# Optimization experiments

Hardware: AMD Instinct MI355X
Metric: run time of the kernel (lower is better)

## Reference

```python
import jax, jax.numpy as jnp
import numpy as np

BN_EPS = 1e-5

def _bn_eval(x, g, b, m, v):
    # BatchNorm1d in eval mode with running stats
    return (x - m) * (g / jnp.sqrt(v + BN_EPS)) + b

def _gcn_layer(x, adj, w, b):
    # D^-0.5 A D^-0.5 (X W) + b  (same math as diag(d^-0.5) @ adj @ diag(d^-0.5))
    deg = adj.sum(axis=1)
    dis = deg ** -0.5
    xw = x @ w
    return dis[:, None] * (adj @ (dis[:, None] * xw)) + b

def setup_inputs() -> dict:
    key = jax.random.key(0)
    ks = jax.random.split(key, 8)
    N, F, E, H, G, C = 16384, 1024, 256, 256, 128, 10
    def xavier(k, i, o):
        s = float(np.sqrt(6.0 / (i + o)))
        return jax.random.uniform(k, (i, o), jnp.float32, -s, s)
    return {
        "feature": jax.random.uniform(ks[0], (N, F), jnp.float32),
        "adj": jax.random.uniform(ks[1], (N, N), jnp.float32),
        "enc_w1": xavier(ks[2], F, 512), "enc_b1": jnp.zeros((512,), jnp.float32),
        "bn1_g": jnp.ones((512,), jnp.float32), "bn1_b": jnp.zeros((512,), jnp.float32),
        "bn1_m": jnp.zeros((512,), jnp.float32), "bn1_v": jnp.ones((512,), jnp.float32),
        "enc_w2": xavier(ks[3], 512, E), "enc_b2": jnp.zeros((E,), jnp.float32),
        "bn2_g": jnp.ones((E,), jnp.float32), "bn2_b": jnp.zeros((E,), jnp.float32),
        "bn2_m": jnp.zeros((E,), jnp.float32), "bn2_v": jnp.ones((E,), jnp.float32),
        "gcn1_w": xavier(ks[4], E, H), "gcn1_b": jnp.zeros((H,), jnp.float32),
        "gcn2_w": xavier(ks[5], H, G), "gcn2_b": jnp.zeros((G,), jnp.float32),
        "cls_w": xavier(ks[6], G, C), "cls_b": jnp.zeros((C,), jnp.float32),
    }

def reference(feature, adj, enc_w1, enc_b1, bn1_g, bn1_b, bn1_m, bn1_v,
              enc_w2, enc_b2, bn2_g, bn2_b, bn2_m, bn2_v,
              gcn1_w, gcn1_b, gcn2_w, gcn2_b, cls_w, cls_b):
    # encoder.encode (eval: dropout off, BN running stats)
    h = jax.nn.relu(_bn_eval(feature @ enc_w1 + enc_b1, bn1_g, bn1_b, bn1_m, bn1_v))
    h = jax.nn.relu(_bn_eval(h @ enc_w2 + enc_b2, bn2_g, bn2_b, bn2_m, bn2_v))
    h = jax.nn.relu(_gcn_layer(h, adj, gcn1_w, gcn1_b))
    h = jax.nn.relu(_gcn_layer(h, adj, gcn2_w, gcn2_b))
    out = jax.nn.sigmoid(h @ cls_w + cls_b)
    return jnp.clip(out, 1e-10, 1 - 1e-10)
```

## Files before the change

kernel.cpp:

```cpp
#include <hip/hip_runtime.h>
#include <stdint.h>

typedef unsigned short u16;
typedef unsigned int u32;
typedef __attribute__((ext_vector_type(4))) float f32x4;
typedef __attribute__((ext_vector_type(16))) float f32x16;
typedef __attribute__((ext_vector_type(8))) short s16x8;
typedef __attribute__((ext_vector_type(4))) short s16x4;
typedef __attribute__((ext_vector_type(2))) unsigned int u32x2;
typedef __attribute__((ext_vector_type(4))) unsigned int u32x4;
typedef __attribute__((ext_vector_type(8))) int i32x8;

__device__ __forceinline__ u16 f2bf(float x){
  unsigned u = __builtin_bit_cast(unsigned, x);
  u += 0x7fffu + ((u >> 16) & 1u);
  return (u16)(u >> 16);
}
__device__ __forceinline__ float bf2f(u16 b){
  return __builtin_bit_cast(float, (unsigned)b << 16);
}
__device__ __forceinline__ u32 pk_fp8x4(float a, float b, float c, float d){
  int w = 0;
  w = __builtin_amdgcn_cvt_pk_fp8_f32(a, b, w, false);
  w = __builtin_amdgcn_cvt_pk_fp8_f32(c, d, w, true);
  return (u32)w;
}


__global__ void bn_prep_kernel(const float* __restrict__ g, const float* __restrict__ b,
                               const float* __restrict__ m, const float* __restrict__ v,
                               const float* __restrict__ lin_b,
                               float* __restrict__ s, float* __restrict__ bb, int n){
  int i = blockIdx.x * 256 + threadIdx.x;
  if (i < n){
    float sc = g[i] * rsqrtf(v[i] + 1e-5f);
    s[i] = sc;
    bb[i] = (lin_b[i] - m[i]) * sc + b[i];
  }
}

__global__ __launch_bounds__(256) void tcvtT_kernel(const float* __restrict__ src,
                                                    u16* __restrict__ dst, int K, int N){
  __shared__ float t[32][33];
  int tx = threadIdx.x & 31, ty = threadIdx.x >> 5;
  int n0 = blockIdx.x * 32, k0 = blockIdx.y * 32;
  #pragma unroll
  for (int i = 0; i < 4; i++)
    t[ty + 8 * i][tx] = src[(size_t)(k0 + ty + 8 * i) * N + n0 + tx];
  __syncthreads();
  #pragma unroll
  for (int i = 0; i < 4; i++)
    dst[(size_t)(n0 + ty + 8 * i) * K + k0 + tx] = f2bf(t[tx][ty + 8 * i]);
}

__global__ __launch_bounds__(256) void enc1_deg_kernel(
    const float* __restrict__ feature, const u16* __restrict__ w1t,
    u16* __restrict__ h1, const float* __restrict__ cs, const float* __restrict__ cb,
    const float* __restrict__ adj, unsigned char* __restrict__ adj8,
    float* __restrict__ dis)
{
  constexpr int BM = 128, BN = 256, BK = 64, WM = 2, WN = 2;
  constexpr int M = 16384, N = 512, K = 1024, NADJ = 16384;
  constexpr int WTM = BM / WM, WTN = BN / WN, FM = WTM / 16, FN = WTN / 16;
  constexpr int AIT = (BM * BK) / (256 * 4);
  constexpr int BIT = (BN * BK) / (256 * 8);

  __shared__ __align__(16) char smem[BM * BK * 2 + BN * BK * 2];

  if (blockIdx.x >= 256){
    int row = blockIdx.x - 256;
    const float* rp = adj + (size_t)row * NADJ;
    unsigned char* wp = adj8 + (size_t)row * NADJ;
    float s = 0.f;
    #pragma unroll
    for (int it = 0; it < 4; ++it){
      const float* p = rp + it * 4096 + threadIdx.x * 16;
      f32x4 v[4];
      #pragma unroll
      for (int j = 0; j < 4; ++j) v[j] = *(const f32x4*)(p + 4 * j);
      u32x4 o;
      #pragma unroll
      for (int j = 0; j < 4; ++j){
        s += (v[j][0] + v[j][1]) + (v[j][2] + v[j][3]);
        o[j] = pk_fp8x4(v[j][0], v[j][1], v[j][2], v[j][3]);
      }
      *(u32x4*)(wp + it * 4096 + threadIdx.x * 16) = o;
    }
    #pragma unroll
    for (int d = 32; d > 0; d >>= 1) s += __shfl_down(s, d, 64);
    float* ps = (float*)smem;
    if ((threadIdx.x & 63) == 0) ps[threadIdx.x >> 6] = s;
    __syncthreads();
    if (threadIdx.x == 0) dis[row] = rsqrtf((ps[0] + ps[1]) + (ps[2] + ps[3]));
    return;
  }

  u16* As = (u16*)smem;
  u16* Bs = (u16*)(smem + BM * BK * 2);
  const int tid = threadIdx.x;
  const int lane = tid & 63;
  const int wid = tid >> 6;
  const int wr = wid / WN;
  const int wc = wid % WN;
  const int bm = (blockIdx.x & 127) * BM;
  const int bn = (blockIdx.x >> 7) * BN;

  f32x4 arf[AIT];
  s16x8 brb[BIT];

  auto load_tiles = [&](int k0){
    #pragma unroll
    for (int i = 0; i < AIT; i++){
      int e = (i * 256 + tid) * 4; int r = e / BK, c = e % BK;
      arf[i] = *(const f32x4*)(feature + (size_t)(bm + r) * K + k0 + c);
    }
    #pragma unroll
    for (int i = 0; i < BIT; i++){
      int e = (i * 256 + tid) * 8; int r = e / BK, c = e % BK;
      brb[i] = *(const s16x8*)(w1t + (size_t)(bn + r) * K + k0 + c);
    }
  };
  auto store_tiles = [&](){
    char* Ac = (char*)As; char* Bc = (char*)Bs;
    #pragma unroll
    for (int i = 0; i < AIT; i++){
      int e = (i * 256 + tid) * 4; int r = e / BK, c = e % BK;
      int off = ((r * BK + c) * 2) ^ ((r & 7) << 4);
      s16x4 o;
      o[0] = (short)f2bf(arf[i][0]); o[1] = (short)f2bf(arf[i][1]);
      o[2] = (short)f2bf(arf[i][2]); o[3] = (short)f2bf(arf[i][3]);
      *(s16x4*)(Ac + off) = o;
    }
    #pragma unroll
    for (int i = 0; i < BIT; i++){
      int e = (i * 256 + tid) * 8; int r = e / BK, c = e % BK;
      int off = ((r * BK + c) * 2) ^ ((r & 7) << 4);
      *(s16x8*)(Bc + off) = brb[i];
    }
  };

  f32x4 acc[FM][FN];
  #pragma unroll
  for (int m = 0; m < FM; m++)
    #pragma unroll
    for (int n = 0; n < FN; n++)
      acc[m][n] = (f32x4){0.f, 0.f, 0.f, 0.f};

  const int arow0 = wr * WTM + (lane & 15);
  const int brow0 = wc * WTN + (lane & 15);
  const int kof = (lane >> 4) * 8;

  load_tiles(0);
  for (int kt = 0; kt < K / BK; ++kt){
    __syncthreads();
    store_tiles();
    __syncthreads();
    if (kt + 1 < K / BK) load_tiles((kt + 1) * BK);
    const char* Ac = (const char*)As;
    const char* Bc = (const char*)Bs;
    #pragma unroll
    for (int ks = 0; ks < BK / 32; ++ks){
      s16x8 af[FM], bfr[FN];
      #pragma unroll
      for (int m = 0; m < FM; m++){
        int r = arow0 + m * 16;
        af[m] = *(const s16x8*)(Ac + (((r * BK + ks * 32 + kof) * 2) ^ ((r & 7) << 4)));
      }
      #pragma unroll
      for (int n = 0; n < FN; n++){
        int r = brow0 + n * 16;
        bfr[n] = *(const s16x8*)(Bc + (((r * BK + ks * 32 + kof) * 2) ^ ((r & 7) << 4)));
      }
      #pragma unroll
      for (int m = 0; m < FM; m++)
        #pragma unroll
        for (int n = 0; n < FN; n++)
          acc[m][n] = __builtin_amdgcn_mfma_f32_16x16x32_bf16(af[m], bfr[n], acc[m][n], 0, 0, 0);
    }
  }
  #pragma unroll
  for (int m = 0; m < FM; m++){
    #pragma unroll
    for (int n = 0; n < FN; n++){
      int col = bn + wc * WTN + n * 16 + (lane & 15);
      int row0 = bm + wr * WTM + m * 16 + (lane >> 4) * 4;
      #pragma unroll
      for (int r4 = 0; r4 < 4; r4++){
        float vv = fmaxf(acc[m][n][r4] * cs[col] + cb[col], 0.f);
        h1[(size_t)(row0 + r4) * N + col] = f2bf(vv);
      }
    }
  }
}

__global__ __launch_bounds__(256) void gcn_reduce_kernel(const float* __restrict__ part,
                                                         const float* __restrict__ dis,
                                                         const float* __restrict__ b,
                                                         u16* __restrict__ out,
                                                         int N, size_t MN, float oscale){
  size_t e4 = ((size_t)blockIdx.x * 256 + threadIdx.x) * 4;
  int row = (int)(e4 / N);
  int col = (int)(e4 % N);
  f32x4 s = *(const f32x4*)(part + e4);
  s += *(const f32x4*)(part + MN + e4);
  float dr = dis[row] * oscale;
  s16x4 o;
  #pragma unroll
  for (int j = 0; j < 4; j++){
    float vv = fmaxf(dr * s[j] + b[col + j], 0.f);
    o[j] = (short)f2bf(vv);
  }
  *(s16x4*)(out + e4) = o;
}

__global__ __launch_bounds__(256) void cls_kernel(const u16* __restrict__ h4,
                                                  const float* __restrict__ w,
                                                  const float* __restrict__ b,
                                                  float* __restrict__ out, int M){
  __shared__ float ws_[128 * 10];
  __shared__ float bs_[10];
  for (int i = threadIdx.x; i < 1280; i += 256) ws_[i] = w[i];
  if (threadIdx.x < 10) bs_[threadIdx.x] = b[threadIdx.x];
  __syncthreads();
  int row = blockIdx.x * 256 + threadIdx.x;
  if (row >= M) return;
  const u16* hp = h4 + (size_t)row * 128;
  float acc[10];
  #pragma unroll
  for (int c = 0; c < 10; c++) acc[c] = bs_[c];
  #pragma unroll
  for (int k8 = 0; k8 < 128; k8 += 8){
    s16x8 hv = *(const s16x8*)(hp + k8);
    #pragma unroll
    for (int j = 0; j < 8; j++){
      float h = bf2f((u16)hv[j]);
      #pragma unroll
      for (int c = 0; c < 10; c++) acc[c] = fmaf(h, ws_[(k8 + j) * 10 + c], acc[c]);
    }
  }
  #pragma unroll
  for (int c = 0; c < 10; c++){
    float sg = 1.f / (1.f + expf(-acc[c]));
    sg = fminf(fmaxf(sg, 1e-10f), 1.f - 1e-10f);
    out[(size_t)row * 10 + c] = sg;
  }
}

template<int BM, int BN>
__global__ __launch_bounds__(512, 1)
void gemm_mx(const unsigned char* __restrict__ A8, const unsigned char* __restrict__ B8,
             float* __restrict__ P, int M, int N, int K, int Ksub)
{
  constexpr int BK = 128;
  constexpr int AT = BM * BK;
  constexpr int BT = BN * BK;
  constexpr int AIT = AT / (512 * 16);
  constexpr int BIT = BT / (512 * 16);
  constexpr int WM = 2, WN = 4;
  constexpr int WTM = BM / WM;
  constexpr int WTN = BN / WN;
  constexpr int FM = WTM / 32;
  constexpr int FN = WTN / 32;
  static_assert(AIT >= 1 && BIT >= 1, "staging");

  __shared__ __align__(16) char LDS[2 * (AT + BT)];

  const int tid = threadIdx.x;
  const int lane = tid & 63;
  const int wid = tid >> 6;
  const int wr = wid >> 2;
  const int wc = wid & 3;
  const int bm = blockIdx.x * BM;
  const int kz = blockIdx.z * Ksub;

  auto stage = [&](int half, int k0){
    char* ab = LDS + half * (AT + BT);
    #pragma unroll
    for (int i = 0; i < AIT; i++){
      int e = (i * 512 + tid) * 16;
      int r = e >> 7, c = e & 127;
      int cc = c ^ ((r & 7) << 4);
      const unsigned char* g = A8 + (size_t)(bm + r) * K + k0 + cc;
      __builtin_amdgcn_global_load_lds((const __attribute__((address_space(1))) unsigned int*)g,
          (__attribute__((address_space(3))) unsigned int*)(ab + e), 16, 0, 0);
    }
    char* bb = ab + AT;
    #pragma unroll
    for (int i = 0; i < BIT; i++){
      int e = (i * 512 + tid) * 16;
      int r = e >> 7, c = e & 127;
      int cc = c ^ ((r & 7) << 4);
      const unsigned char* g = B8 + (size_t)r * K + k0 + cc;
      __builtin_amdgcn_global_load_lds((const __attribute__((address_space(1))) unsigned int*)g,
          (__attribute__((address_space(3))) unsigned int*)(bb + e), 16, 0, 0);
    }
  };

  f32x16 acc[FM][FN];
  #pragma unroll
  for (int m = 0; m < FM; m++)
    #pragma unroll
    for (int n = 0; n < FN; n++)
      #pragma unroll
      for (int i = 0; i < 16; i++)
        acc[m][n][i] = 0.f;

  const int nk = Ksub / BK;
  stage(0, kz);
  for (int kt = 0; kt < nk; ++kt){
    __syncthreads();
    if (kt + 1 < nk) stage((kt + 1) & 1, kz + (kt + 1) * BK);
    const char* ab = LDS + (kt & 1) * (AT + BT);
    const char* bb = ab + AT;
    #pragma unroll
    for (int ks = 0; ks < 2; ks++){
      const int c0 = ks * 64 + (lane >> 5) * 32;
      i32x8 af[FM], bf_[FN];
      #pragma unroll
      for (int m = 0; m < FM; m++){
        int r = wr * WTM + m * 32 + (lane & 31);
        int sw = (r & 7) << 4;
        int o = r * BK + c0;
        u32x4 lo = *(const u32x4*)(ab + (o ^ sw));
        u32x4 hi = *(const u32x4*)(ab + ((o + 16) ^ sw));
        af[m][0] = lo[0]; af[m][1] = lo[1]; af[m][2] = lo[2]; af[m][3] = lo[3];
        af[m][4] = hi[0]; af[m][5] = hi[1]; af[m][6] = hi[2]; af[m][7] = hi[3];
      }
      #pragma unroll
      for (int n = 0; n < FN; n++){
        int r = wc * WTN + n * 32 + (lane & 31);
        int sw = (r & 7) << 4;
        int o = r * BK + c0;
        u32x4 lo = *(const u32x4*)(bb + (o ^ sw));
        u32x4 hi = *(const u32x4*)(bb + ((o + 16) ^ sw));
        bf_[n][0] = lo[0]; bf_[n][1] = lo[1]; bf_[n][2] = lo[2]; bf_[n][3] = lo[3];
        bf_[n][4] = hi[0]; bf_[n][5] = hi[1]; bf_[n][6] = hi[2]; bf_[n][7] = hi[3];
      }
      #pragma unroll
      for (int m = 0; m < FM; m++)
        #pragma unroll
        for (int n = 0; n < FN; n++)
          acc[m][n] = __builtin_amdgcn_mfma_scale_f32_32x32x64_f8f6f4(
              af[m], bf_[n], acc[m][n], 0, 0, 0, 0x7F7F7F7F, 0, 0x7F7F7F7F);
    }
  }

  float* Pz = P + (size_t)blockIdx.z * M * N;
  #pragma unroll
  for (int m = 0; m < FM; m++){
    #pragma unroll
    for (int n = 0; n < FN; n++){
      int colg = wc * WTN + n * 32 + (lane & 31);
      int rbase = bm + wr * WTM + m * 32 + (lane >> 5) * 4;
      #pragma unroll
      for (int i = 0; i < 16; i++){
        int rowg = rbase + (i & 3) + 8 * (i >> 2);
        Pz[(size_t)rowg * N + colg] = acc[m][n][i];
      }
    }
  }
}

enum { EPI_BNRELU = 0, EPI_SCALET = 1 };

template<int BM, int BN, int BK, int WM, int WN, int EPI>
__global__ __launch_bounds__(WM*WN*64, 1)
void gemm_k(const u16* __restrict__ Ab, const u16* __restrict__ Bb,
            void* __restrict__ Cp, int M, int N, int K,
            const float* __restrict__ cs, const float* __restrict__ cb,
            const float* __restrict__ rs, float oscale)
{
  constexpr int NT = WM * WN * 64;
  constexpr int WTM = BM / WM;
  constexpr int WTN = BN / WN;
  constexpr int FM = WTM / 16;
  constexpr int FN = WTN / 16;
  constexpr int AIT = (BM * BK) / (NT * 8);
  constexpr int BIT = (BN * BK) / (NT * 8);
  static_assert((BM * BK) % (NT * 8) == 0, "A staging");
  static_assert((BN * BK) % (NT * 8) == 0, "B staging");

  __shared__ u16 As[BM * BK];
  __shared__ u16 Bs[BN * BK];

  const int tid = threadIdx.x;
  const int lane = tid & 63;
  const int wid = tid >> 6;
  const int wr = wid / WN;
  const int wc = wid % WN;
  const int bm = blockIdx.x * BM;
  const int bn = blockIdx.y * BN;

  s16x8 arb[AIT];
  s16x8 brb[BIT];

  auto load_tiles = [&](int k0){
    #pragma unroll
    for (int i = 0; i < AIT; i++){
      int e = (i * NT + tid) * 8; int r = e / BK, c = e % BK;
      arb[i] = *(const s16x8*)(Ab + (size_t)(bm + r) * K + k0 + c);
    }
    #pragma unroll
    for (int i = 0; i < BIT; i++){
      int e = (i * NT + tid) * 8; int r = e / BK, c = e % BK;
      brb[i] = *(const s16x8*)(Bb + (size_t)(bn + r) * K + k0 + c);
    }
  };
  auto store_tiles = [&](){
    char* Ac = (char*)As; char* Bc = (char*)Bs;
    #pragma unroll
    for (int i = 0; i < AIT; i++){
      int e = (i * NT + tid) * 8; int r = e / BK, c = e % BK;
      int off = ((r * BK + c) * 2) ^ ((r & 7) << 4);
      *(s16x8*)(Ac + off) = arb[i];
    }
    #pragma unroll
    for (int i = 0; i < BIT; i++){
      int e = (i * NT + tid) * 8; int r = e / BK, c = e % BK;
      int off = ((r * BK + c) * 2) ^ ((r & 7) << 4);
      *(s16x8*)(Bc + off) = brb[i];
    }
  };

  f32x4 acc[FM][FN];
  #pragma unroll
  for (int m = 0; m < FM; m++)
    #pragma unroll
    for (int n = 0; n < FN; n++)
      acc[m][n] = (f32x4){0.f, 0.f, 0.f, 0.f};

  const int arow0 = wr * WTM + (lane & 15);
  const int brow0 = wc * WTN + (lane & 15);
  const int kof = (lane >> 4) * 8;

  const int nk = K / BK;
  load_tiles(0);
  for (int kt = 0; kt < nk; ++kt){
    __syncthreads();
    store_tiles();
    __syncthreads();
    if (kt + 1 < nk) load_tiles((kt + 1) * BK);
    const char* Ac = (const char*)As;
    const char* Bc = (const char*)Bs;
    #pragma unroll
    for (int ks = 0; ks < BK / 32; ++ks){
      s16x8 af[FM], bfr[FN];
      #pragma unroll
      for (int m = 0; m < FM; m++){
        int r = arow0 + m * 16;
        af[m] = *(const s16x8*)(Ac + (((r * BK + ks * 32 + kof) * 2) ^ ((r & 7) << 4)));
      }
      #pragma unroll
      for (int n = 0; n < FN; n++){
        int r = brow0 + n * 16;
        bfr[n] = *(const s16x8*)(Bc + (((r * BK + ks * 32 + kof) * 2) ^ ((r & 7) << 4)));
      }
      #pragma unroll
      for (int m = 0; m < FM; m++)
        #pragma unroll
        for (int n = 0; n < FN; n++)
          acc[m][n] = __builtin_amdgcn_mfma_f32_16x16x32_bf16(af[m], bfr[n], acc[m][n], 0, 0, 0);
    }
  }

  #pragma unroll
  for (int m = 0; m < FM; m++){
    #pragma unroll
    for (int n = 0; n < FN; n++){
      int col = bn + wc * WTN + n * 16 + (lane & 15);
      int row0 = bm + wr * WTM + m * 16 + (lane >> 4) * 4;
      if constexpr (EPI == EPI_SCALET){
        float v0 = acc[m][n][0] * rs[row0 + 0] * oscale;
        float v1 = acc[m][n][1] * rs[row0 + 1] * oscale;
        float v2 = acc[m][n][2] * rs[row0 + 2] * oscale;
        float v3 = acc[m][n][3] * rs[row0 + 3] * oscale;
        *(u32*)((unsigned char*)Cp + (size_t)col * M + row0) = pk_fp8x4(v0, v1, v2, v3);
      } else {
        #pragma unroll
        for (int r4 = 0; r4 < 4; r4++){
          int row = row0 + r4;
          float vv = fmaxf(acc[m][n][r4] * cs[col] + cb[col], 0.f);
          ((u16*)Cp)[(size_t)row * N + col] = f2bf(vv);
        }
      }
    }
  }
}


extern "C" void kernel_launch(void* const* d_in, const int* in_sizes, int n_in,
                              void* d_out, int out_size, void* d_ws, size_t ws_size,
                              hipStream_t stream)
{
  (void)in_sizes; (void)n_in; (void)out_size; (void)ws_size;
  const float* feature = (const float*)d_in[0];
  const float* adj     = (const float*)d_in[1];
  const float* enc_w1  = (const float*)d_in[2];
  const float* enc_b1  = (const float*)d_in[3];
  const float* bn1_g   = (const float*)d_in[4];
  const float* bn1_b   = (const float*)d_in[5];
  const float* bn1_m   = (const float*)d_in[6];
  const float* bn1_v   = (const float*)d_in[7];
  const float* enc_w2  = (const float*)d_in[8];
  const float* enc_b2  = (const float*)d_in[9];
  const float* bn2_g   = (const float*)d_in[10];
  const float* bn2_b   = (const float*)d_in[11];
  const float* bn2_m   = (const float*)d_in[12];
  const float* bn2_v   = (const float*)d_in[13];
  const float* gcn1_w  = (const float*)d_in[14];
  const float* gcn1_b  = (const float*)d_in[15];
  const float* gcn2_w  = (const float*)d_in[16];
  const float* gcn2_b  = (const float*)d_in[17];
  const float* cls_w   = (const float*)d_in[18];
  const float* cls_b   = (const float*)d_in[19];
  float* out = (float*)d_out;

  const int NN = 16384, F = 1024, H1 = 512, E = 256, H = 256, G = 128;
  const float SC = 256.f, SCI = 1.f / 256.f;

  char* ws = (char*)d_ws;
  size_t off = 0;
  auto alloc = [&](size_t bytes) -> char* {
    char* p = ws + off; off += (bytes + 255) & ~(size_t)255; return p;
  };
  float* dis = (float*)alloc((size_t)NN * 4);
  float* s1  = (float*)alloc((size_t)H1 * 4);
  float* bb1 = (float*)alloc((size_t)H1 * 4);
  float* s2  = (float*)alloc((size_t)E * 4);
  float* bb2 = (float*)alloc((size_t)E * 4);
  u16* w1t = (u16*)alloc((size_t)H1 * F * 2);
  u16* w2t = (u16*)alloc((size_t)E * H1 * 2);
  u16* g1t = (u16*)alloc((size_t)H * E * 2);
  u16* g2t = (u16*)alloc((size_t)G * H * 2);
  u16* h1  = (u16*)alloc((size_t)NN * H1 * 2);
  u16* h2  = (u16*)alloc((size_t)NN * E * 2);
  unsigned char* tT  = (unsigned char*)alloc((size_t)E * NN);
  u16* h3  = (u16*)alloc((size_t)NN * H * 2);
  unsigned char* t2T = (unsigned char*)alloc((size_t)G * NN);
  u16* h4  = (u16*)alloc((size_t)NN * G * 2);
  float* part = (float*)alloc((size_t)2 * NN * H * 4);
  unsigned char* adj8 = (unsigned char*)alloc((size_t)NN * NN);

  bn_prep_kernel<<<(H1 + 255) / 256, 256, 0, stream>>>(bn1_g, bn1_b, bn1_m, bn1_v, enc_b1, s1, bb1, H1);
  bn_prep_kernel<<<(E + 255) / 256, 256, 0, stream>>>(bn2_g, bn2_b, bn2_m, bn2_v, enc_b2, s2, bb2, E);
  tcvtT_kernel<<<dim3(H1/32, F/32), 256, 0, stream>>>(enc_w1, w1t, F, H1);
  tcvtT_kernel<<<dim3(E/32, H1/32), 256, 0, stream>>>(enc_w2, w2t, H1, E);
  tcvtT_kernel<<<dim3(H/32, E/32), 256, 0, stream>>>(gcn1_w, g1t, E, H);
  tcvtT_kernel<<<dim3(G/32, H/32), 256, 0, stream>>>(gcn2_w, g2t, H, G);

  enc1_deg_kernel<<<256 + NN, 256, 0, stream>>>(feature, w1t, h1, s1, bb1, adj, adj8, dis);

  gemm_k<128,128,64,2,2,EPI_BNRELU><<<dim3(NN/128, E/128), 256, 0, stream>>>(
      h1, w2t, h2, NN, E, H1, s2, bb2, nullptr, 1.f);
  gemm_k<128,128,64,2,2,EPI_SCALET><<<dim3(NN/128, H/128), 256, 0, stream>>>(
      h2, g1t, tT, NN, H, E, nullptr, nullptr, dis, SC);
  gemm_mx<128,256><<<dim3(NN/128, 1, 2), 512, 0, stream>>>(
      adj8, tT, part, NN, H, NN, NN/2);
  gcn_reduce_kernel<<<(NN * H) / 1024, 256, 0, stream>>>(
      part, dis, gcn1_b, h3, H, (size_t)NN * H, SCI);
  gemm_k<64,128,64,2,2,EPI_SCALET><<<dim3(NN/64, G/128), 256, 0, stream>>>(
      h3, g2t, t2T, NN, G, H, nullptr, nullptr, dis, SC);
  gemm_mx<128,128><<<dim3(NN/128, 1, 2), 512, 0, stream>>>(
      adj8, t2T, part, NN, G, NN, NN/2);
  gcn_reduce_kernel<<<(NN * G) / 1024, 256, 0, stream>>>(
      part, dis, gcn2_b, h4, G, (size_t)NN * G, SCI);
  cls_kernel<<<NN/256, 256, 0, stream>>>(h4, cls_w, cls_b, out, NN);
}
```

Baseline: 520.4 us.

## Fuse prep, small GEMMs, split-K reductions and classifier into fewer kernels

```diff
diff --git a/kernel.cpp b/kernel.cpp
--- a/kernel.cpp
+++ b/kernel.cpp
@@ -27,11 +27,26 @@
 }
 
 
-__global__ void bn_prep_kernel(const float* __restrict__ g, const float* __restrict__ b,
-                               const float* __restrict__ m, const float* __restrict__ v,
-                               const float* __restrict__ lin_b,
-                               float* __restrict__ s, float* __restrict__ bb, int n){
-  int i = blockIdx.x * 256 + threadIdx.x;
+__device__ __forceinline__ void tcvtT_dev(const float* __restrict__ src, u16* __restrict__ dst,
+                                          int K, int N, int bx, int by, char* smem){
+  float (*t)[33] = (float (*)[33])smem;
+  int tx = threadIdx.x & 31, ty = threadIdx.x >> 5;
+  int n0 = bx * 32, k0 = by * 32;
+  #pragma unroll
+  for (int i = 0; i < 4; i++)
+    t[ty + 8 * i][tx] = src[(size_t)(k0 + ty + 8 * i) * N + n0 + tx];
+  __syncthreads();
+  #pragma unroll
+  for (int i = 0; i < 4; i++)
+    dst[(size_t)(n0 + ty + 8 * i) * K + k0 + tx] = f2bf(t[tx][ty + 8 * i]);
+}
+
+__device__ __forceinline__ void bn_dev(const float* __restrict__ g, const float* __restrict__ b,
+                                       const float* __restrict__ m, const float* __restrict__ v,
+                                       const float* __restrict__ lin_b,
+                                       float* __restrict__ s, float* __restrict__ bb,
+                                       int n, int blk){
+  int i = blk * 256 + threadIdx.x;
   if (i < n){
     float sc = g[i] * rsqrtf(v[i] + 1e-5f);
     s[i] = sc;
@@ -39,33 +54,47 @@
   }
 }
 
-__global__ __launch_bounds__(256) void tcvtT_kernel(const float* __restrict__ src,
-                                                    u16* __restrict__ dst, int K, int N){
-  __shared__ float t[32][33];
-  int tx = threadIdx.x & 31, ty = threadIdx.x >> 5;
-  int n0 = blockIdx.x * 32, k0 = blockIdx.y * 32;
-  #pragma unroll
-  for (int i = 0; i < 4; i++)
-    t[ty + 8 * i][tx] = src[(size_t)(k0 + ty + 8 * i) * N + n0 + tx];
-  __syncthreads();
-  #pragma unroll
-  for (int i = 0; i < 4; i++)
-    dst[(size_t)(n0 + ty + 8 * i) * K + k0 + tx] = f2bf(t[tx][ty + 8 * i]);
+__global__ __launch_bounds__(256) void prep0_kernel(
+    const float* __restrict__ enc_w1, u16* __restrict__ w1t,
+    const float* __restrict__ g, const float* __restrict__ b,
+    const float* __restrict__ m, const float* __restrict__ v,
+    const float* __restrict__ lin_b, float* __restrict__ s1, float* __restrict__ bb1)
+{
+  __shared__ char smem[32 * 33 * 4 + 64];
+  if (blockIdx.x < 512)
+    tcvtT_dev(enc_w1, w1t, 1024, 512, blockIdx.x & 15, blockIdx.x >> 4, smem);
+  else
+    bn_dev(g, b, m, v, lin_b, s1, bb1, 512, blockIdx.x - 512);
 }
 
 __global__ __launch_bounds__(256) void enc1_deg_kernel(
     const float* __restrict__ feature, const u16* __restrict__ w1t,
     u16* __restrict__ h1, const float* __restrict__ cs, const float* __restrict__ cb,
     const float* __restrict__ adj, unsigned char* __restrict__ adj8,
-    float* __restrict__ dis)
+    float* __restrict__ dis,
+    const float* __restrict__ enc_w2, u16* __restrict__ w2t,
+    const float* __restrict__ gcn1_w, u16* __restrict__ g1t,
+    const float* __restrict__ gcn2_w, u16* __restrict__ g2t,
+    const float* __restrict__ bn2_g, const float* __restrict__ bn2_b,
+    const float* __restrict__ bn2_m, const float* __restrict__ bn2_v,
+    const float* __restrict__ enc_b2, float* __restrict__ s2, float* __restrict__ bb2)
 {
   constexpr int BM = 128, BN = 256, BK = 64, WM = 2, WN = 2;
-  constexpr int M = 16384, N = 512, K = 1024, NADJ = 16384;
+  constexpr int N = 512, K = 1024, NADJ = 16384;
   constexpr int WTM = BM / WM, WTN = BN / WN, FM = WTM / 16, FN = WTN / 16;
   constexpr int AIT = (BM * BK) / (256 * 4);
   constexpr int BIT = (BN * BK) / (256 * 8);
 
   __shared__ __align__(16) char smem[BM * BK * 2 + BN * BK * 2];
+
+  if (blockIdx.x >= 16640){
+    int p = blockIdx.x - 16640;
+    if (p < 128)       tcvtT_dev(enc_w2, w2t, 512, 256, p & 7, p >> 3, smem);
+    else if (p < 192){ int l = p - 128; tcvtT_dev(gcn1_w, g1t, 256, 256, l & 7, l >> 3, smem); }
+    else if (p < 224){ int l = p - 192; tcvtT_dev(gcn2_w, g2t, 256, 128, l & 3, l >> 2, smem); }
+    else               bn_dev(bn2_g, bn2_b, bn2_m, bn2_v, enc_b2, s2, bb2, 256, 0);
+    return;
+  }
 
   if (blockIdx.x >= 256){
     int row = blockIdx.x - 256;
@@ -193,56 +222,173 @@
   }
 }
 
-__global__ __launch_bounds__(256) void gcn_reduce_kernel(const float* __restrict__ part,
-                                                         const float* __restrict__ dis,
-                                                         const float* __restrict__ b,
-                                                         u16* __restrict__ out,
-                                                         int N, size_t MN, float oscale){
-  size_t e4 = ((size_t)blockIdx.x * 256 + threadIdx.x) * 4;
-  int row = (int)(e4 / N);
-  int col = (int)(e4 % N);
-  f32x4 s = *(const f32x4*)(part + e4);
-  s += *(const f32x4*)(part + MN + e4);
-  float dr = dis[row] * oscale;
-  s16x4 o;
-  #pragma unroll
-  for (int j = 0; j < 4; j++){
-    float vv = fmaxf(dr * s[j] + b[col + j], 0.f);
-    o[j] = (short)f2bf(vv);
-  }
-  *(s16x4*)(out + e4) = o;
-}
-
-__global__ __launch_bounds__(256) void cls_kernel(const u16* __restrict__ h4,
-                                                  const float* __restrict__ w,
-                                                  const float* __restrict__ b,
-                                                  float* __restrict__ out, int M){
-  __shared__ float ws_[128 * 10];
-  __shared__ float bs_[10];
-  for (int i = threadIdx.x; i < 1280; i += 256) ws_[i] = w[i];
-  if (threadIdx.x < 10) bs_[threadIdx.x] = b[threadIdx.x];
-  __syncthreads();
-  int row = blockIdx.x * 256 + threadIdx.x;
-  if (row >= M) return;
-  const u16* hp = h4 + (size_t)row * 128;
-  float acc[10];
-  #pragma unroll
-  for (int c = 0; c < 10; c++) acc[c] = bs_[c];
-  #pragma unroll
-  for (int k8 = 0; k8 < 128; k8 += 8){
-    s16x8 hv = *(const s16x8*)(hp + k8);
-    #pragma unroll
-    for (int j = 0; j < 8; j++){
-      float h = bf2f((u16)hv[j]);
-      #pragma unroll
-      for (int c = 0; c < 10; c++) acc[c] = fmaf(h, ws_[(k8 + j) * 10 + c], acc[c]);
-    }
-  }
-  #pragma unroll
-  for (int c = 0; c < 10; c++){
-    float sg = 1.f / (1.f + expf(-acc[c]));
-    sg = fminf(fmaxf(sg, 1e-10f), 1.f - 1e-10f);
-    out[(size_t)row * 10 + c] = sg;
+__global__ __launch_bounds__(256, 1)
+void h2tT_kernel(const u16* __restrict__ h1, const u16* __restrict__ w2t,
+                 const float* __restrict__ s2, const float* __restrict__ bb2,
+                 const u16* __restrict__ g1t, const float* __restrict__ dis,
+                 unsigned char* __restrict__ tT)
+{
+  constexpr int M = 16384, K1 = 512, E = 256, K2 = 256, BK = 64;
+  constexpr float SC = 256.f;
+
+  __shared__ u16 As[64 * BK];
+  __shared__ u16 Bs[256 * BK];
+  __shared__ u16 H2s[64 * 256];
+
+  const int tid = threadIdx.x;
+  const int lane = tid & 63;
+  const int wc = tid >> 6;
+  const int bm = blockIdx.x * 64;
+  const int arow0 = lane & 15;
+  const int kof = (lane >> 4) * 8;
+
+  {
+    s16x8 arb[2], brb[8];
+    auto load1 = [&](int k0){
+      #pragma unroll
+      for (int i = 0; i < 2; i++){
+        int e = (i * 256 + tid) * 8; int r = e >> 6, c = e & 63;
+        arb[i] = *(const s16x8*)(h1 + (size_t)(bm + r) * K1 + k0 + c);
+      }
+      #pragma unroll
+      for (int i = 0; i < 8; i++){
+        int e = (i * 256 + tid) * 8; int r = e >> 6, c = e & 63;
+        brb[i] = *(const s16x8*)(w2t + (size_t)r * K1 + k0 + c);
+      }
+    };
+    auto store1 = [&](){
+      char* Ac = (char*)As; char* Bc = (char*)Bs;
+      #pragma unroll
+      for (int i = 0; i < 2; i++){
+        int e = (i * 256 + tid) * 8; int r = e >> 6, c = e & 63;
+        *(s16x8*)(Ac + (((r * BK + c) * 2) ^ ((r & 7) << 4))) = arb[i];
+      }
+      #pragma unroll
+      for (int i = 0; i < 8; i++){
+        int e = (i * 256 + tid) * 8; int r = e >> 6, c = e & 63;
+        *(s16x8*)(Bc + (((r * BK + c) * 2) ^ ((r & 7) << 4))) = brb[i];
+      }
+    };
+
+    f32x4 acc[4][4];
+    #pragma unroll
+    for (int m = 0; m < 4; m++)
+      #pragma unroll
+      for (int n = 0; n < 4; n++)
+        acc[m][n] = (f32x4){0.f, 0.f, 0.f, 0.f};
+
+    load1(0);
+    for (int kt = 0; kt < K1 / BK; ++kt){
+      __syncthreads();
+      store1();
+      __syncthreads();
+      if (kt + 1 < K1 / BK) load1((kt + 1) * BK);
+      const char* Ac = (const char*)As;
+      const char* Bc = (const char*)Bs;
+      #pragma unroll
+      for (int ks = 0; ks < 2; ++ks){
+        s16x8 af[4], bfr[4];
+        #pragma unroll
+        for (int m = 0; m < 4; m++){
+          int r = arow0 + m * 16;
+          af[m] = *(const s16x8*)(Ac + (((r * BK + ks * 32 + kof) * 2) ^ ((r & 7) << 4)));
+        }
+        #pragma unroll
+        for (int n = 0; n < 4; n++){
+          int r = wc * 64 + n * 16 + (lane & 15);
+          bfr[n] = *(const s16x8*)(Bc + (((r * BK + ks * 32 + kof) * 2) ^ ((r & 7) << 4)));
+        }
+        #pragma unroll
+        for (int m = 0; m < 4; m++)
+          #pragma unroll
+          for (int n = 0; n < 4; n++)
+            acc[m][n] = __builtin_amdgcn_mfma_f32_16x16x32_bf16(af[m], bfr[n], acc[m][n], 0, 0, 0);
+      }
+    }
+    __syncthreads();
+    char* Hc = (char*)H2s;
+    #pragma unroll
+    for (int m = 0; m < 4; m++){
+      #pragma unroll
+      for (int n = 0; n < 4; n++){
+        int col = wc * 64 + n * 16 + (lane & 15);
+        int row0 = m * 16 + (lane >> 4) * 4;
+        #pragma unroll
+        for (int r4 = 0; r4 < 4; r4++){
+          int row = row0 + r4;
+          float vv = fmaxf(acc[m][n][r4] * s2[col] + bb2[col], 0.f);
+          *(u16*)(Hc + (((row * 256 + col) * 2) ^ ((row & 7) << 4))) = f2bf(vv);
+        }
+      }
+    }
+  }
+
+  {
+    s16x8 brb[8];
+    auto load2 = [&](int k0){
+      #pragma unroll
+      for (int i = 0; i < 8; i++){
+        int e = (i * 256 + tid) * 8; int r = e >> 6, c = e & 63;
+        brb[i] = *(const s16x8*)(g1t + (size_t)r * K2 + k0 + c);
+      }
+    };
+    auto store2 = [&](){
+      char* Bc = (char*)Bs;
+      #pragma unroll
+      for (int i = 0; i < 8; i++){
+        int e = (i * 256 + tid) * 8; int r = e >> 6, c = e & 63;
+        *(s16x8*)(Bc + (((r * BK + c) * 2) ^ ((r & 7) << 4))) = brb[i];
+      }
+    };
+
+    f32x4 acc[4][4];
+    #pragma unroll
+    for (int m = 0; m < 4; m++)
+      #pragma unroll
+      for (int n = 0; n < 4; n++)
+        acc[m][n] = (f32x4){0.f, 0.f, 0.f, 0.f};
+
+    load2(0);
+    for (int kt = 0; kt < K2 / BK; ++kt){
+      __syncthreads();
+      store2();
+      __syncthreads();
+      if (kt + 1 < K2 / BK) load2((kt + 1) * BK);
+      const char* Hc = (const char*)H2s;
+      const char* Bc = (const char*)Bs;
+      #pragma unroll
+      for (int ks = 0; ks < 2; ++ks){
+        s16x8 af[4], bfr[4];
+        #pragma unroll
+        for (int m = 0; m < 4; m++){
+          int r = arow0 + m * 16;
+          af[m] = *(const s16x8*)(Hc + (((r * 256 + kt * 64 + ks * 32 + kof) * 2) ^ ((r & 7) << 4)));
+        }
+        #pragma unroll
+        for (int n = 0; n < 4; n++){
+          int r = wc * 64 + n * 16 + (lane & 15);
+          bfr[n] = *(const s16x8*)(Bc + (((r * BK + ks * 32 + kof) * 2) ^ ((r & 7) << 4)));
+        }
+        #pragma unroll
+        for (int m = 0; m < 4; m++)
+          #pragma unroll
+          for (int n = 0; n < 4; n++)
+            acc[m][n] = __builtin_amdgcn_mfma_f32_16x16x32_bf16(af[m], bfr[n], acc[m][n], 0, 0, 0);
+      }
+    }
+    #pragma unroll
+    for (int m = 0; m < 4; m++){
+      #pragma unroll
+      for (int n = 0; n < 4; n++){
+        int col = wc * 64 + n * 16 + (lane & 15);
+        int row0 = bm + m * 16 + (lane >> 4) * 4;
+        float v0 = acc[m][n][0] * dis[row0 + 0] * SC;
+        float v1 = acc[m][n][1] * dis[row0 + 1] * SC;
+        float v2 = acc[m][n][2] * dis[row0 + 2] * SC;
+        float v3 = acc[m][n][3] * dis[row0 + 3] * SC;
+        *(u32*)(tT + (size_t)col * M + row0) = pk_fp8x4(v0, v1, v2, v3);
+      }
+    }
   }
 }
 
@@ -361,129 +507,161 @@
   }
 }
 
-enum { EPI_BNRELU = 0, EPI_SCALET = 1 };
-
-template<int BM, int BN, int BK, int WM, int WN, int EPI>
-__global__ __launch_bounds__(WM*WN*64, 1)
-void gemm_k(const u16* __restrict__ Ab, const u16* __restrict__ Bb,
-            void* __restrict__ Cp, int M, int N, int K,
-            const float* __restrict__ cs, const float* __restrict__ cb,
-            const float* __restrict__ rs, float oscale)
+__global__ __launch_bounds__(256, 1)
+void t2g_kernel(const float* __restrict__ part, const float* __restrict__ dis,
+                const float* __restrict__ g1b, const u16* __restrict__ g2t,
+                unsigned char* __restrict__ t2T)
 {
-  constexpr int NT = WM * WN * 64;
-  constexpr int WTM = BM / WM;
-  constexpr int WTN = BN / WN;
-  constexpr int FM = WTM / 16;
-  constexpr int FN = WTN / 16;
-  constexpr int AIT = (BM * BK) / (NT * 8);
-  constexpr int BIT = (BN * BK) / (NT * 8);
-  static_assert((BM * BK) % (NT * 8) == 0, "A staging");
-  static_assert((BN * BK) % (NT * 8) == 0, "B staging");
-
-  __shared__ u16 As[BM * BK];
-  __shared__ u16 Bs[BN * BK];
+  constexpr int M = 16384, H = 256, BK = 64;
+  constexpr float SC = 256.f, SCI = 1.f / 256.f;
+  const size_t MN = (size_t)M * H;
+
+  __shared__ u16 As[64 * BK];
+  __shared__ u16 Bs[128 * BK];
 
   const int tid = threadIdx.x;
   const int lane = tid & 63;
   const int wid = tid >> 6;
-  const int wr = wid / WN;
-  const int wc = wid % WN;
-  const int bm = blockIdx.x * BM;
-  const int bn = blockIdx.y * BN;
-
-  s16x8 arb[AIT];
-  s16x8 brb[BIT];
+  const int wr = wid >> 1;
+  const int wc = wid & 1;
+  const int bm = blockIdx.x * 64;
+  const int kof = (lane >> 4) * 8;
+
+  f32x4 a0r[4], a1r[4], gbr[4];
+  float dsr[4];
+  s16x8 brb[4];
 
   auto load_tiles = [&](int k0){
     #pragma unroll
-    for (int i = 0; i < AIT; i++){
-      int e = (i * NT + tid) * 8; int r = e / BK, c = e % BK;
-      arb[i] = *(const s16x8*)(Ab + (size_t)(bm + r) * K + k0 + c);
-    }
-    #pragma unroll
-    for (int i = 0; i < BIT; i++){
-      int e = (i * NT + tid) * 8; int r = e / BK, c = e % BK;
-      brb[i] = *(const s16x8*)(Bb + (size_t)(bn + r) * K + k0 + c);
+    for (int i = 0; i < 4; i++){
+      int e = (i * 256 + tid) * 4; int r = e >> 6, c = e & 63;
+      size_t pi = (size_t)(bm + r) * H + k0 + c;
+      a0r[i] = *(const f32x4*)(part + pi);
+      a1r[i] = *(const f32x4*)(part + MN + pi);
+      gbr[i] = *(const f32x4*)(g1b + k0 + c);
+      dsr[i] = dis[bm + r];
+    }
+    #pragma unroll
+    for (int i = 0; i < 4; i++){
+      int e = (i * 256 + tid) * 8; int r = e >> 6, c = e & 63;
+      brb[i] = *(const s16x8*)(g2t + (size_t)r * H + k0 + c);
     }
   };
   auto store_tiles = [&](){
     char* Ac = (char*)As; char* Bc = (char*)Bs;
     #pragma unroll
-    for (int i = 0; i < AIT; i++){
-      int e = (i * NT + tid) * 8; int r = e / BK, c = e % BK;
-      int off = ((r * BK + c) * 2) ^ ((r & 7) << 4);
-      *(s16x8*)(Ac + off) = arb[i];
-    }
-    #pragma unroll
-    for (int i = 0; i < BIT; i++){
-      int e = (i * NT + tid) * 8; int r = e / BK, c = e % BK;
-      int off = ((r * BK + c) * 2) ^ ((r & 7) << 4);
-      *(s16x8*)(Bc + off) = brb[i];
+    for (int i = 0; i < 4; i++){
+      int e = (i * 256 + tid) * 4; int r = e >> 6, c = e & 63;
+      float dsc = dsr[i] * SCI;
+      s16x4 o;
+      #pragma unroll
+      for (int j = 0; j < 4; j++){
+        float vv = fmaxf(dsc * (a0r[i][j] + a1r[i][j]) + gbr[i][j], 0.f);
+        o[j] = (short)f2bf(vv);
+      }
+      *(s16x4*)(Ac + (((r * BK + c) * 2) ^ ((r & 7) << 4))) = o;
+    }
+    #pragma unroll
+    for (int i = 0; i < 4; i++){
+      int e = (i * 256 + tid) * 8; int r = e >> 6, c = e & 63;
+      *(s16x8*)(Bc + (((r * BK + c) * 2) ^ ((r & 7) << 4))) = brb[i];
     }
   };
 
-  f32x4 acc[FM][FN];
-  #pragma unroll
-  for (int m = 0; m < FM; m++)
-    #pragma unroll
-    for (int n = 0; n < FN; n++)
+  f32x4 acc[2][4];
+  #pragma unroll
+  for (int m = 0; m < 2; m++)
+    #pragma unroll
+    for (int n = 0; n < 4; n++)
       acc[m][n] = (f32x4){0.f, 0.f, 0.f, 0.f};
 
-  const int arow0 = wr * WTM + (lane & 15);
-  const int brow0 = wc * WTN + (lane & 15);
-  const int kof = (lane >> 4) * 8;
-
-  const int nk = K / BK;
   load_tiles(0);
-  for (int kt = 0; kt < nk; ++kt){
+  for (int kt = 0; kt < H / BK; ++kt){
     __syncthreads();
     store_tiles();
     __syncthreads();
-    if (kt + 1 < nk) load_tiles((kt + 1) * BK);
+    if (kt + 1 < H / BK) load_tiles((kt + 1) * BK);
     const char* Ac = (const char*)As;
     const char* Bc = (const char*)Bs;
     #pragma unroll
-    for (int ks = 0; ks < BK / 32; ++ks){
-      s16x8 af[FM], bfr[FN];
-      #pragma unroll
-      for (int m = 0; m < FM; m++){
-        int r = arow0 + m * 16;
+    for (int ks = 0; ks < 2; ++ks){
+      s16x8 af[2], bfr[4];
+      #pragma unroll
+      for (int m = 0; m < 2; m++){
+        int r = wr * 32 + m * 16 + (lane & 15);
         af[m] = *(const s16x8*)(Ac + (((r * BK + ks * 32 + kof) * 2) ^ ((r & 7) << 4)));
       }
       #pragma unroll
-      for (int n = 0; n < FN; n++){
-        int r = brow0 + n * 16;
+      for (int n = 0; n < 4; n++){
+        int r = wc * 64 + n * 16 + (lane & 15);
         bfr[n] = *(const s16x8*)(Bc + (((r * BK + ks * 32 + kof) * 2) ^ ((r & 7) << 4)));
       }
       #pragma unroll
-      for (int m = 0; m < FM; m++)
-        #pragma unroll
-        for (int n = 0; n < FN; n++)
+      for (int m = 0; m < 2; m++)
+        #pragma unroll
+        for (int n = 0; n < 4; n++)
           acc[m][n] = __builtin_amdgcn_mfma_f32_16x16x32_bf16(af[m], bfr[n], acc[m][n], 0, 0, 0);
     }
   }
 
   #pragma unroll
-  for (int m = 0; m < FM; m++){
-    #pragma unroll
-    for (int n = 0; n < FN; n++){
-      int col = bn + wc * WTN + n * 16 + (lane & 15);
-      int row0 = bm + wr * WTM + m * 16 + (lane >> 4) * 4;
-      if constexpr (EPI == EPI_SCALET){
-        float v0 = acc[m][n][0] * rs[row0 + 0] * oscale;
-        float v1 = acc[m][n][1] * rs[row0 + 1] * oscale;
-        float v2 = acc[m][n][2] * rs[row0 + 2] * oscale;
-        float v3 = acc[m][n][3] * rs[row0 + 3] * oscale;
-        *(u32*)((unsigned char*)Cp + (size_t)col * M + row0) = pk_fp8x4(v0, v1, v2, v3);
-      } else {
-        #pragma unroll
-        for (int r4 = 0; r4 < 4; r4++){
-          int row = row0 + r4;
-          float vv = fmaxf(acc[m][n][r4] * cs[col] + cb[col], 0.f);
-          ((u16*)Cp)[(size_t)row * N + col] = f2bf(vv);
-        }
-      }
-    }
+  for (int m = 0; m < 2; m++){
+    #pragma unroll
+    for (int n = 0; n < 4; n++){
+      int col = wc * 64 + n * 16 + (lane & 15);
+      int row0 = bm + wr * 32 + m * 16 + (lane >> 4) * 4;
+      float v0 = acc[m][n][0] * dis[row0 + 0] * SC;
+      float v1 = acc[m][n][1] * dis[row0 + 1] * SC;
+      float v2 = acc[m][n][2] * dis[row0 + 2] * SC;
+      float v3 = acc[m][n][3] * dis[row0 + 3] * SC;
+      *(u32*)(t2T + (size_t)col * M + row0) = pk_fp8x4(v0, v1, v2, v3);
+    }
+  }
+}
+
+__global__ __launch_bounds__(256) void cls2_kernel(const float* __restrict__ part,
+                                                   const float* __restrict__ dis,
+                                                   const float* __restrict__ g2b,
+                                                   const float* __restrict__ w,
+                                                   const float* __restrict__ b,
+                                                   float* __restrict__ out)
+{
+  constexpr int M = 16384, G = 128;
+  constexpr float SCI = 1.f / 256.f;
+  const size_t MN = (size_t)M * G;
+  __shared__ float ws_[G * 10];
+  __shared__ float bs_[10];
+  __shared__ float gb_[G];
+  for (int i = threadIdx.x; i < G * 10; i += 256) ws_[i] = w[i];
+  if (threadIdx.x < 10) bs_[threadIdx.x] = b[threadIdx.x];
+  if (threadIdx.x < G) gb_[threadIdx.x] = g2b[threadIdx.x];
+  __syncthreads();
+  int row = blockIdx.x * 256 + threadIdx.x;
+  const float* p0 = part + (size_t)row * G;
+  const float* p1 = p0 + MN;
+  float dr = dis[row] * SCI;
+  float acc[10];
+  #pragma unroll
+  for (int c = 0; c < 10; c++) acc[c] = bs_[c];
+  for (int k16 = 0; k16 < G; k16 += 16){
+    f32x4 a0[4], a1[4];
+    #pragma unroll
+    for (int j = 0; j < 4; j++){
+      a0[j] = *(const f32x4*)(p0 + k16 + 4 * j);
+      a1[j] = *(const f32x4*)(p1 + k16 + 4 * j);
+    }
+    #pragma unroll
+    for (int j = 0; j < 16; j++){
+      float h = fmaxf(dr * (a0[j >> 2][j & 3] + a1[j >> 2][j & 3]) + gb_[k16 + j], 0.f);
+      #pragma unroll
+      for (int c = 0; c < 10; c++) acc[c] = fmaf(h, ws_[(k16 + j) * 10 + c], acc[c]);
+    }
+  }
+  #pragma unroll
+  for (int c = 0; c < 10; c++){
+    float sg = 1.f / (1.f + expf(-acc[c]));
+    sg = fminf(fmaxf(sg, 1e-10f), 1.f - 1e-10f);
+    out[(size_t)row * 10 + c] = sg;
   }
 }
 
@@ -516,7 +694,6 @@
   float* out = (float*)d_out;
 
   const int NN = 16384, F = 1024, H1 = 512, E = 256, H = 256, G = 128;
-  const float SC = 256.f, SCI = 1.f / 256.f;
 
   char* ws = (char*)d_ws;
   size_t off = 0;
@@ -533,36 +710,27 @@
   u16* g1t = (u16*)alloc((size_t)H * E * 2);
   u16* g2t = (u16*)alloc((size_t)G * H * 2);
   u16* h1  = (u16*)alloc((size_t)NN * H1 * 2);
-  u16* h2  = (u16*)alloc((size_t)NN * E * 2);
   unsigned char* tT  = (unsigned char*)alloc((size_t)E * NN);
-  u16* h3  = (u16*)alloc((size_t)NN * H * 2);
   unsigned char* t2T = (unsigned char*)alloc((size_t)G * NN);
-  u16* h4  = (u16*)alloc((size_t)NN * G * 2);
   float* part = (float*)alloc((size_t)2 * NN * H * 4);
   unsigned char* adj8 = (unsigned char*)alloc((size_t)NN * NN);
 
-  bn_prep_kernel<<<(H1 + 255) / 256, 256, 0, stream>>>(bn1_g, bn1_b, bn1_m, bn1_v, enc_b1, s1, bb1, H1);
-  bn_prep_kernel<<<(E + 255) / 256, 256, 0, stream>>>(bn2_g, bn2_b, bn2_m, bn2_v, enc_b2, s2, bb2, E);
-  tcvtT_kernel<<<dim3(H1/32, F/32), 256, 0, stream>>>(enc_w1, w1t, F, H1);
-  tcvtT_kernel<<<dim3(E/32, H1/32), 256, 0, stream>>>(enc_w2, w2t, H1, E);
-  tcvtT_kernel<<<dim3(H/32, E/32), 256, 0, stream>>>(gcn1_w, g1t, E, H);
-  tcvtT_kernel<<<dim3(G/32, H/32), 256, 0, stream>>>(gcn2_w, g2t, H, G);
-
-  enc1_deg_kernel<<<256 + NN, 256, 0, stream>>>(feature, w1t, h1, s1, bb1, adj, adj8, dis);
-
-  gemm_k<128,128,64,2,2,EPI_BNRELU><<<dim3(NN/128, E/128), 256, 0, stream>>>(
-      h1, w2t, h2, NN, E, H1, s2, bb2, nullptr, 1.f);
-  gemm_k<128,128,64,2,2,EPI_SCALET><<<dim3(NN/128, H/128), 256, 0, stream>>>(
-      h2, g1t, tT, NN, H, E, nullptr, nullptr, dis, SC);
+  prep0_kernel<<<514, 256, 0, stream>>>(enc_w1, w1t, bn1_g, bn1_b, bn1_m, bn1_v, enc_b1, s1, bb1);
+
+  enc1_deg_kernel<<<256 + NN + 225, 256, 0, stream>>>(
+      feature, w1t, h1, s1, bb1, adj, adj8, dis,
+      enc_w2, w2t, gcn1_w, g1t, gcn2_w, g2t,
+      bn2_g, bn2_b, bn2_m, bn2_v, enc_b2, s2, bb2);
+
+  h2tT_kernel<<<NN / 64, 256, 0, stream>>>(h1, w2t, s2, bb2, g1t, dis, tT);
+
   gemm_mx<128,256><<<dim3(NN/128, 1, 2), 512, 0, stream>>>(
       adj8, tT, part, NN, H, NN, NN/2);
-  gcn_reduce_kernel<<<(NN * H) / 1024, 256, 0, stream>>>(
-      part, dis, gcn1_b, h3, H, (size_t)NN * H, SCI);
-  gemm_k<64,128,64,2,2,EPI_SCALET><<<dim3(NN/64, G/128), 256, 0, stream>>>(
-      h3, g2t, t2T, NN, G, H, nullptr, nullptr, dis, SC);
+
+  t2g_kernel<<<NN / 64, 256, 0, stream>>>(part, dis, gcn1_b, g2t, t2T);
+
   gemm_mx<128,128><<<dim3(NN/128, 1, 2), 512, 0, stream>>>(
       adj8, t2T, part, NN, G, NN, NN/2);
-  gcn_reduce_kernel<<<(NN * G) / 1024, 256, 0, stream>>>(
-      part, dis, gcn2_b, h4, G, (size_t)NN * G, SCI);
-  cls_kernel<<<NN/256, 256, 0, stream>>>(h4, cls_w, cls_b, out, NN);
-}
+
+  cls2_kernel<<<NN / 256, 256, 0, stream>>>(part, dis, gcn2_b, cls_w, cls_b, out);
+}
```

Result: faster. 494.9 us (-4.9%).
